# Optimization experiments

Measured on AMD Instinct MI355X. Metric: run time of the kernel, lower is better.

## Reference

```python
import jax, jax.numpy as jnp
import numpy as np

D, C, H, W = 8, 512, 64, 64


def setup_inputs() -> dict:
    key = jax.random.key(0)
    k1, k2, k3 = jax.random.split(key, 3)
    x = jax.random.normal(k1, (D, C, H, W), dtype=jnp.float32)
    atten = jax.random.normal(k2, (D, C, C), dtype=jnp.float32)
    gamma = jax.random.normal(k3, (1,), dtype=jnp.float32)
    return {"x": x, "atten": atten, "gamma": gamma}


def reference(x, atten, gamma):
    d, c, h, w = x.shape
    q = x.reshape(d, c, h * w)              # q == v == flattened x; k = q^T
    # energy[d, i, j] = <channel_i, channel_j> over spatial positions
    energy = jnp.einsum('din,djn->dij', q, q)
    # max-centering: rowmax - energy (note the sign flip vs standard softmax)
    energy_new = jnp.max(energy, axis=-1, keepdims=True) - energy
    attention = jax.nn.softmax(energy_new, axis=-1)
    attention = jax.nn.softmax(attention + atten, axis=-1)
    # out = attention^T @ v : out[d, j, n] = sum_i attention[d, i, j] * v[d, i, n]
    out = jnp.einsum('dij,din->djn', attention, q).reshape(d, c, h, w)
    return gamma * out + x
```

## Files before the change

kernel.cpp:

```cpp
#include <hip/hip_runtime.h>
#include <hip/hip_bf16.h>

#define DD 8
#define CC 512
#define NN 4096
#define SPLITK 4
#define KSP (NN / SPLITK)

typedef __bf16 bf16x8 __attribute__((ext_vector_type(8)));
typedef float  f32x4  __attribute__((ext_vector_type(4)));

__device__ __forceinline__ ushort f2bf(float f) {
  unsigned u = __float_as_uint(f);
  u = (u + 0x7fffu + ((u >> 16) & 1u)) >> 16;
  return (ushort)u;
}
__device__ __forceinline__ float bf2f(ushort h) {
  return __uint_as_float(((unsigned)h) << 16);
}

__device__ __forceinline__ void gl_lds16(const ushort* g, ushort* l) {
  __builtin_amdgcn_global_load_lds(
      (const __attribute__((address_space(1))) void*)g,
      (__attribute__((address_space(3))) void*)l, 16, 0, 0);
}

__global__ __launch_bounds__(256) void k0_convert(
    const float* __restrict__ x, ushort* __restrict__ qh,
    ushort* __restrict__ ql, ushort* __restrict__ qt) {
  int d = blockIdx.z, ct = blockIdx.y, nt = blockIdx.x;
  __shared__ ushort T[64][68];
  int t = threadIdx.x;
  int rr = t >> 4;
  int c4 = (t & 15) * 4;
  const float* xb = x + ((size_t)(d * CC + ct * 64)) * NN + nt * 64;
#pragma unroll
  for (int it = 0; it < 4; ++it) {
    int r = it * 16 + rr;
    float4 v = *(const float4*)(xb + (size_t)r * NN + c4);
    ushort h0 = f2bf(v.x), h1 = f2bf(v.y), h2 = f2bf(v.z), h3 = f2bf(v.w);
    ushort l0 = f2bf(v.x - bf2f(h0)), l1 = f2bf(v.y - bf2f(h1));
    ushort l2 = f2bf(v.z - bf2f(h2)), l3 = f2bf(v.w - bf2f(h3));
    size_t qi = ((size_t)(d * CC + ct * 64 + r)) * NN + nt * 64 + c4;
    *(ushort4*)(qh + qi) = make_ushort4(h0, h1, h2, h3);
    *(ushort4*)(ql + qi) = make_ushort4(l0, l1, l2, l3);
    *(ushort4*)&T[r][c4] = make_ushort4(h0, h1, h2, h3);
  }
  __syncthreads();
#pragma unroll
  for (int it = 0; it < 4; ++it) {
    int nl = it * 16 + rr;
    ushort4 v = make_ushort4(T[c4 + 0][nl], T[c4 + 1][nl], T[c4 + 2][nl], T[c4 + 3][nl]);
    *(ushort4*)(qt + ((size_t)(d * NN + nt * 64 + nl)) * CC + ct * 64 + c4) = v;
  }
}

__global__ __launch_bounds__(256, 2) void k1_gram(
    const ushort* __restrict__ qh, const ushort* __restrict__ ql,
    float* __restrict__ Ep) {
  __shared__ ushort As[2][128 * 32];
  __shared__ ushort Bs[2][128 * 32];
  int b = blockIdx.x;
  int s = b & 3, tmn = (b >> 2) & 15, d = b >> 6;
  int tm = tmn >> 2, tn = tmn & 3;
  int t = threadIdx.x, lane = t & 63, w = t >> 6;
  int wm = (w >> 1) * 64, wn = (w & 1) * 64;
  int qd = lane >> 4, fr = lane & 15;

  const ushort* srcbase = (w & 1) ? ql : qh;
  int rowblk = (w < 2) ? tm : tn;
  const ushort* gsrc = srcbase +
      ((size_t)(d * CC + rowblk * 128 + (lane >> 2))) * NN +
      (size_t)s * KSP + (lane & 3) * 8;
  ushort* ldst = (w < 2) ? As[w & 1] : Bs[w & 1];

  f32x4 acc[4][4];
#pragma unroll
  for (int i = 0; i < 4; ++i)
#pragma unroll
    for (int j = 0; j < 4; ++j) acc[i][j] = (f32x4){0.f, 0.f, 0.f, 0.f};

  for (int kk = 0; kk < KSP / 32; ++kk) {
    __syncthreads();
    const ushort* g0 = gsrc + (size_t)kk * 32;
#pragma unroll
    for (int c = 0; c < 8; ++c)
      gl_lds16(g0 + (size_t)c * 16 * NN, ldst + c * 512);
    __syncthreads();

    bf16x8 ah[4], al[4];
#pragma unroll
    for (int mi = 0; mi < 4; ++mi) {
      int off = (wm + mi * 16 + fr) * 32 + qd * 8;
      ah[mi] = *(const bf16x8*)&As[0][off];
      al[mi] = *(const bf16x8*)&As[1][off];
    }
#pragma unroll
    for (int ni = 0; ni < 4; ++ni) {
      int off = (wn + ni * 16 + fr) * 32 + qd * 8;
      bf16x8 bh = *(const bf16x8*)&Bs[0][off];
      bf16x8 bl = *(const bf16x8*)&Bs[1][off];
#pragma unroll
      for (int mi = 0; mi < 4; ++mi) {
        acc[mi][ni] = __builtin_amdgcn_mfma_f32_16x16x32_bf16(ah[mi], bh, acc[mi][ni], 0, 0, 0);
        acc[mi][ni] = __builtin_amdgcn_mfma_f32_16x16x32_bf16(ah[mi], bl, acc[mi][ni], 0, 0, 0);
        acc[mi][ni] = __builtin_amdgcn_mfma_f32_16x16x32_bf16(al[mi], bh, acc[mi][ni], 0, 0, 0);
      }
    }
  }

  size_t ebase = ((size_t)(s * DD + d)) * ((size_t)CC * CC);
#pragma unroll
  for (int mi = 0; mi < 4; ++mi) {
    int r0 = tm * 128 + wm + mi * 16 + qd * 4;
#pragma unroll
    for (int ni = 0; ni < 4; ++ni) {
      int c0 = tn * 128 + wn + ni * 16 + fr;
      float* ep = Ep + ebase + (size_t)r0 * CC + c0;
#pragma unroll
      for (int r = 0; r < 4; ++r) ep[(size_t)r * CC] = acc[mi][ni][r];
    }
  }
}

__device__ __forceinline__ float bred(float v, float* red, int op) {
#pragma unroll
  for (int o = 32; o > 0; o >>= 1) {
    float other = __shfl_xor(v, o, 64);
    v = (op == 0) ? fminf(v, other) : (op == 1) ? (v + other) : fmaxf(v, other);
  }
  __syncthreads();
  if ((threadIdx.x & 63) == 0) red[threadIdx.x >> 6] = v;
  __syncthreads();
  if (op == 0) return fminf(fminf(red[0], red[1]), fminf(red[2], red[3]));
  if (op == 1) return red[0] + red[1] + red[2] + red[3];
  return fmaxf(fmaxf(red[0], red[1]), fmaxf(red[2], red[3]));
}

__global__ __launch_bounds__(256) void k2_softmax(
    const float* __restrict__ Ep, const float* __restrict__ atten,
    ushort* __restrict__ a2t) {
  int d = blockIdx.y, i0 = blockIdx.x * 16;
  int t = threadIdx.x;
  __shared__ float red[4];
  __shared__ ushort T[512][17];
  const size_t SP = (size_t)DD * CC * CC;
  for (int r = 0; r < 16; ++r) {
    size_t base = ((size_t)(d * CC + i0 + r)) * CC;
    float e0 = Ep[base + t] + Ep[SP + base + t] + Ep[2 * SP + base + t] + Ep[3 * SP + base + t];
    float e1 = Ep[base + t + 256] + Ep[SP + base + t + 256] +
               Ep[2 * SP + base + t + 256] + Ep[3 * SP + base + t + 256];
    float mn = bred(fminf(e0, e1), red, 0);
    float p0 = __expf(mn - e0), p1 = __expf(mn - e1);
    float s1 = bred(p0 + p1, red, 1);
    float inv1 = 1.0f / s1;
    float t0 = p0 * inv1 + atten[base + t];
    float t1 = p1 * inv1 + atten[base + t + 256];
    float mx = bred(fmaxf(t0, t1), red, 2);
    float q0 = __expf(t0 - mx), q1 = __expf(t1 - mx);
    float s2 = bred(q0 + q1, red, 1);
    float inv2 = 1.0f / s2;
    T[t][r] = f2bf(q0 * inv2);
    T[t + 256][r] = f2bf(q1 * inv2);
  }
  __syncthreads();
#pragma unroll
  for (int jj = 0; jj < 2; ++jj) {
    int j = t + jj * 256;
    size_t ob = ((size_t)(d * CC + j)) * CC + i0;
#pragma unroll
    for (int c4 = 0; c4 < 4; ++c4) {
      ushort4 v = make_ushort4(T[j][c4 * 4], T[j][c4 * 4 + 1],
                               T[j][c4 * 4 + 2], T[j][c4 * 4 + 3]);
      *(ushort4*)(a2t + ob + c4 * 4) = v;
    }
  }
}

__global__ __launch_bounds__(256, 2) void k3_out(
    const ushort* __restrict__ a2t, const ushort* __restrict__ qt,
    const float* __restrict__ x, const float* __restrict__ gamma,
    float* __restrict__ out) {
  __shared__ ushort As[128 * 32];
  __shared__ ushort Bs[128 * 32];
  int b = blockIdx.x;
  int nt = b & 31, jt = (b >> 5) & 3, d = b >> 7;
  int t = threadIdx.x, lane = t & 63, w = t >> 6;
  int wm = (w >> 1) * 64, wn = (w & 1) * 64;
  int qd = lane >> 4, fr = lane & 15;

  const ushort* src = (w < 2)
      ? (a2t + (size_t)d * CC * CC + (size_t)(jt * 128) * CC)
      : (qt + (size_t)d * NN * CC + (size_t)(nt * 128) * CC);
  ushort* ldst = (w < 2) ? As : Bs;
  int cbase = (w & 1) * 4;
  const ushort* g0 = src + ((size_t)(cbase * 16 + (lane >> 2))) * CC + (lane & 3) * 8;
  ushort* l0 = ldst + cbase * 16 * 32;

  f32x4 acc[4][4];
#pragma unroll
  for (int i = 0; i < 4; ++i)
#pragma unroll
    for (int j = 0; j < 4; ++j) acc[i][j] = (f32x4){0.f, 0.f, 0.f, 0.f};

  for (int kk = 0; kk < CC / 32; ++kk) {
    __syncthreads();
#pragma unroll
    for (int c = 0; c < 4; ++c)
      gl_lds16(g0 + kk * 32 + (size_t)(c * 16) * CC, l0 + c * 512);
    __syncthreads();

    bf16x8 a[4];
#pragma unroll
    for (int mi = 0; mi < 4; ++mi)
      a[mi] = *(const bf16x8*)&As[(wm + mi * 16 + fr) * 32 + qd * 8];
#pragma unroll
    for (int ni = 0; ni < 4; ++ni) {
      bf16x8 bb = *(const bf16x8*)&Bs[(wn + ni * 16 + fr) * 32 + qd * 8];
#pragma unroll
      for (int mi = 0; mi < 4; ++mi)
        acc[mi][ni] = __builtin_amdgcn_mfma_f32_16x16x32_bf16(a[mi], bb, acc[mi][ni], 0, 0, 0);
    }
  }

  float g = gamma[0];
#pragma unroll
  for (int mi = 0; mi < 4; ++mi) {
    int j0 = jt * 128 + wm + mi * 16 + qd * 4;
#pragma unroll
    for (int ni = 0; ni < 4; ++ni) {
      int n0 = nt * 128 + wn + ni * 16 + fr;
#pragma unroll
      for (int r = 0; r < 4; ++r) {
        size_t idx = ((size_t)(d * CC + j0 + r)) * NN + n0;
        out[idx] = g * acc[mi][ni][r] + x[idx];
      }
    }
  }
}

extern "C" void kernel_launch(void* const* d_in, const int* in_sizes, int n_in,
                              void* d_out, int out_size, void* d_ws, size_t ws_size,
                              hipStream_t stream) {
  (void)in_sizes; (void)n_in; (void)out_size; (void)ws_size;
  const float* x     = (const float*)d_in[0];
  const float* atten = (const float*)d_in[1];
  const float* gamma = (const float*)d_in[2];
  float* out = (float*)d_out;

  char* ws = (char*)d_ws;
  ushort* qh  = (ushort*)(ws);
  ushort* ql  = (ushort*)(ws + 33554432);
  ushort* qt  = (ushort*)(ws + 67108864);
  float*  Ep  = (float*) (ws + 100663296);
  ushort* a2t = (ushort*)(ws + 134217728);

  k0_convert<<<dim3(64, 8, 8), 256, 0, stream>>>(x, qh, ql, qt);
  k1_gram   <<<dim3(512), 256, 0, stream>>>(qh, ql, Ep);
  k2_softmax<<<dim3(32, 8), 256, 0, stream>>>(Ep, atten, a2t);
  k3_out    <<<dim3(1024), 256, 0, stream>>>(a2t, qt, x, gamma, out);
}
```

Measured before the change: 256.6 us.

## Exploit Gram symmetry, adaptive split-K, warp-per-row softmax, vectorized output epilogue

The Gram kernel now computes only the 10 upper-triangular 128x128 tiles per batch and mirrors off-diagonal tiles with a transposed write, roughly halving MFMA work. Split-K depth becomes a runtime parameter, going to 8 when the workspace is large enough, to keep more blocks in flight. The softmax kernel handles one row per wavefront with 8 elements per lane, so it reduces with shuffles only and no block barriers, and it uses vector loads and stores. The output GEMM swaps operand roles so the epilogue does float4 loads of x and float4 stores of out. The costs are more partial-sum traffic when split is 8 and scattered transposed writes for the mirrored tiles.

Result: faster. 235.0 us (-8.4%).

```diff
diff --git a/kernel.cpp b/kernel.cpp
--- a/kernel.cpp
+++ b/kernel.cpp
@@ -4,11 +4,10 @@
 #define DD 8
 #define CC 512
 #define NN 4096
-#define SPLITK 4
-#define KSP (NN / SPLITK)
 
 typedef __bf16 bf16x8 __attribute__((ext_vector_type(8)));
 typedef float  f32x4  __attribute__((ext_vector_type(4)));
+typedef ushort ush8   __attribute__((ext_vector_type(8)));
 
 __device__ __forceinline__ ushort f2bf(float f) {
   unsigned u = __float_as_uint(f);
@@ -57,12 +56,15 @@
 
 __global__ __launch_bounds__(256, 2) void k1_gram(
     const ushort* __restrict__ qh, const ushort* __restrict__ ql,
-    float* __restrict__ Ep) {
+    float* __restrict__ Ep, int ns, int nkk, int ksp) {
   __shared__ ushort As[2][128 * 32];
   __shared__ ushort Bs[2][128 * 32];
   int b = blockIdx.x;
-  int s = b & 3, tmn = (b >> 2) & 15, d = b >> 6;
-  int tm = tmn >> 2, tn = tmn & 3;
+  int s = b % ns;
+  int rem = b / ns;
+  int tile = rem % 10, d = rem / 10;
+  int tm = (int)((0x3221110000ULL >> (tile * 4)) & 15ULL);
+  int tn = (int)((0x3323213210ULL >> (tile * 4)) & 15ULL);
   int t = threadIdx.x, lane = t & 63, w = t >> 6;
   int wm = (w >> 1) * 64, wn = (w & 1) * 64;
   int qd = lane >> 4, fr = lane & 15;
@@ -71,7 +73,7 @@
   int rowblk = (w < 2) ? tm : tn;
   const ushort* gsrc = srcbase +
       ((size_t)(d * CC + rowblk * 128 + (lane >> 2))) * NN +
-      (size_t)s * KSP + (lane & 3) * 8;
+      (size_t)s * ksp + (lane & 3) * 8;
   ushort* ldst = (w < 2) ? As[w & 1] : Bs[w & 1];
 
   f32x4 acc[4][4];
@@ -80,7 +82,7 @@
 #pragma unroll
     for (int j = 0; j < 4; ++j) acc[i][j] = (f32x4){0.f, 0.f, 0.f, 0.f};
 
-  for (int kk = 0; kk < KSP / 32; ++kk) {
+  for (int kk = 0; kk < nkk; ++kk) {
     __syncthreads();
     const ushort* g0 = gsrc + (size_t)kk * 32;
 #pragma unroll
@@ -121,59 +123,96 @@
       for (int r = 0; r < 4; ++r) ep[(size_t)r * CC] = acc[mi][ni][r];
     }
   }
-}
-
-__device__ __forceinline__ float bred(float v, float* red, int op) {
-#pragma unroll
-  for (int o = 32; o > 0; o >>= 1) {
-    float other = __shfl_xor(v, o, 64);
-    v = (op == 0) ? fminf(v, other) : (op == 1) ? (v + other) : fmaxf(v, other);
-  }
-  __syncthreads();
-  if ((threadIdx.x & 63) == 0) red[threadIdx.x >> 6] = v;
-  __syncthreads();
-  if (op == 0) return fminf(fminf(red[0], red[1]), fminf(red[2], red[3]));
-  if (op == 1) return red[0] + red[1] + red[2] + red[3];
-  return fmaxf(fmaxf(red[0], red[1]), fmaxf(red[2], red[3]));
+  if (tm != tn) {
+#pragma unroll
+    for (int mi = 0; mi < 4; ++mi) {
+      int r0 = tm * 128 + wm + mi * 16 + qd * 4;
+#pragma unroll
+      for (int ni = 0; ni < 4; ++ni) {
+        int c0 = tn * 128 + wn + ni * 16 + fr;
+        float4 v = make_float4(acc[mi][ni][0], acc[mi][ni][1],
+                               acc[mi][ni][2], acc[mi][ni][3]);
+        *(float4*)(Ep + ebase + (size_t)c0 * CC + r0) = v;
+      }
+    }
+  }
+}
+
+__device__ __forceinline__ float wmin(float v) {
+#pragma unroll
+  for (int o = 32; o > 0; o >>= 1) v = fminf(v, __shfl_xor(v, o));
+  return v;
+}
+__device__ __forceinline__ float wmax(float v) {
+#pragma unroll
+  for (int o = 32; o > 0; o >>= 1) v = fmaxf(v, __shfl_xor(v, o));
+  return v;
+}
+__device__ __forceinline__ float wsum(float v) {
+#pragma unroll
+  for (int o = 32; o > 0; o >>= 1) v += __shfl_xor(v, o);
+  return v;
 }
 
 __global__ __launch_bounds__(256) void k2_softmax(
     const float* __restrict__ Ep, const float* __restrict__ atten,
-    ushort* __restrict__ a2t) {
-  int d = blockIdx.y, i0 = blockIdx.x * 16;
-  int t = threadIdx.x;
-  __shared__ float red[4];
-  __shared__ ushort T[512][17];
+    ushort* __restrict__ a2t, int ns) {
+  int d = blockIdx.y, i0 = blockIdx.x * 8;
+  int t = threadIdx.x, lane = t & 63, w = t >> 6;
+  int j8 = lane * 8;
+  __shared__ ushort T[8][520];
   const size_t SP = (size_t)DD * CC * CC;
-  for (int r = 0; r < 16; ++r) {
-    size_t base = ((size_t)(d * CC + i0 + r)) * CC;
-    float e0 = Ep[base + t] + Ep[SP + base + t] + Ep[2 * SP + base + t] + Ep[3 * SP + base + t];
-    float e1 = Ep[base + t + 256] + Ep[SP + base + t + 256] +
-               Ep[2 * SP + base + t + 256] + Ep[3 * SP + base + t + 256];
-    float mn = bred(fminf(e0, e1), red, 0);
-    float p0 = __expf(mn - e0), p1 = __expf(mn - e1);
-    float s1 = bred(p0 + p1, red, 1);
+
+#pragma unroll
+  for (int r2 = 0; r2 < 2; ++r2) {
+    int ri = w * 2 + r2;
+    size_t base = ((size_t)(d * CC + i0 + ri)) * CC + j8;
+    f32x4 a0 = (f32x4){0.f, 0.f, 0.f, 0.f};
+    f32x4 a1 = (f32x4){0.f, 0.f, 0.f, 0.f};
+    for (int s = 0; s < ns; ++s) {
+      const float* p = Ep + (size_t)s * SP + base;
+      a0 += *(const f32x4*)p;
+      a1 += *(const f32x4*)(p + 4);
+    }
+    float mn = fminf(fminf(fminf(a0[0], a0[1]), fminf(a0[2], a0[3])),
+                     fminf(fminf(a1[0], a1[1]), fminf(a1[2], a1[3])));
+    mn = wmin(mn);
+    float p0 = __expf(mn - a0[0]), p1 = __expf(mn - a0[1]);
+    float p2 = __expf(mn - a0[2]), p3 = __expf(mn - a0[3]);
+    float p4 = __expf(mn - a1[0]), p5 = __expf(mn - a1[1]);
+    float p6 = __expf(mn - a1[2]), p7 = __expf(mn - a1[3]);
+    float s1 = wsum(p0 + p1 + p2 + p3 + p4 + p5 + p6 + p7);
     float inv1 = 1.0f / s1;
-    float t0 = p0 * inv1 + atten[base + t];
-    float t1 = p1 * inv1 + atten[base + t + 256];
-    float mx = bred(fmaxf(t0, t1), red, 2);
-    float q0 = __expf(t0 - mx), q1 = __expf(t1 - mx);
-    float s2 = bred(q0 + q1, red, 1);
+    const float* ap = atten + base;
+    f32x4 t0 = *(const f32x4*)ap;
+    f32x4 t1 = *(const f32x4*)(ap + 4);
+    float u0 = p0 * inv1 + t0[0], u1 = p1 * inv1 + t0[1];
+    float u2 = p2 * inv1 + t0[2], u3 = p3 * inv1 + t0[3];
+    float u4 = p4 * inv1 + t1[0], u5 = p5 * inv1 + t1[1];
+    float u6 = p6 * inv1 + t1[2], u7 = p7 * inv1 + t1[3];
+    float mx = wmax(fmaxf(fmaxf(fmaxf(u0, u1), fmaxf(u2, u3)),
+                          fmaxf(fmaxf(u4, u5), fmaxf(u6, u7))));
+    float q0 = __expf(u0 - mx), q1 = __expf(u1 - mx);
+    float q2 = __expf(u2 - mx), q3 = __expf(u3 - mx);
+    float q4 = __expf(u4 - mx), q5 = __expf(u5 - mx);
+    float q6 = __expf(u6 - mx), q7 = __expf(u7 - mx);
+    float s2 = wsum(q0 + q1 + q2 + q3 + q4 + q5 + q6 + q7);
     float inv2 = 1.0f / s2;
-    T[t][r] = f2bf(q0 * inv2);
-    T[t + 256][r] = f2bf(q1 * inv2);
+    ush8 o;
+    o[0] = f2bf(q0 * inv2); o[1] = f2bf(q1 * inv2);
+    o[2] = f2bf(q2 * inv2); o[3] = f2bf(q3 * inv2);
+    o[4] = f2bf(q4 * inv2); o[5] = f2bf(q5 * inv2);
+    o[6] = f2bf(q6 * inv2); o[7] = f2bf(q7 * inv2);
+    *(ush8*)&T[ri][j8] = o;
   }
   __syncthreads();
 #pragma unroll
-  for (int jj = 0; jj < 2; ++jj) {
-    int j = t + jj * 256;
-    size_t ob = ((size_t)(d * CC + j)) * CC + i0;
-#pragma unroll
-    for (int c4 = 0; c4 < 4; ++c4) {
-      ushort4 v = make_ushort4(T[j][c4 * 4], T[j][c4 * 4 + 1],
-                               T[j][c4 * 4 + 2], T[j][c4 * 4 + 3]);
-      *(ushort4*)(a2t + ob + c4 * 4) = v;
-    }
+  for (int it = 0; it < 2; ++it) {
+    int j = t + it * 256;
+    ush8 o;
+#pragma unroll
+    for (int k = 0; k < 8; ++k) o[k] = T[k][j];
+    *(ush8*)&a2t[((size_t)(d * CC + j)) * CC + i0] = o;
   }
 }
 
@@ -186,7 +225,7 @@
   int b = blockIdx.x;
   int nt = b & 31, jt = (b >> 5) & 3, d = b >> 7;
   int t = threadIdx.x, lane = t & 63, w = t >> 6;
-  int wm = (w >> 1) * 64, wn = (w & 1) * 64;
+  int wj = (w >> 1) * 64, wn2 = (w & 1) * 64;
   int qd = lane >> 4, fr = lane & 15;
 
   const ushort* src = (w < 2)
@@ -210,31 +249,33 @@
       gl_lds16(g0 + kk * 32 + (size_t)(c * 16) * CC, l0 + c * 512);
     __syncthreads();
 
-    bf16x8 a[4];
-#pragma unroll
-    for (int mi = 0; mi < 4; ++mi)
-      a[mi] = *(const bf16x8*)&As[(wm + mi * 16 + fr) * 32 + qd * 8];
-#pragma unroll
-    for (int ni = 0; ni < 4; ++ni) {
-      bf16x8 bb = *(const bf16x8*)&Bs[(wn + ni * 16 + fr) * 32 + qd * 8];
-#pragma unroll
-      for (int mi = 0; mi < 4; ++mi)
-        acc[mi][ni] = __builtin_amdgcn_mfma_f32_16x16x32_bf16(a[mi], bb, acc[mi][ni], 0, 0, 0);
+    bf16x8 qf[4];
+#pragma unroll
+    for (int ii = 0; ii < 4; ++ii)
+      qf[ii] = *(const bf16x8*)&Bs[(wn2 + ii * 16 + fr) * 32 + qd * 8];
+#pragma unroll
+    for (int jj = 0; jj < 4; ++jj) {
+      bf16x8 af = *(const bf16x8*)&As[(wj + jj * 16 + fr) * 32 + qd * 8];
+#pragma unroll
+      for (int ii = 0; ii < 4; ++ii)
+        acc[ii][jj] = __builtin_amdgcn_mfma_f32_16x16x32_bf16(qf[ii], af, acc[ii][jj], 0, 0, 0);
     }
   }
 
   float g = gamma[0];
 #pragma unroll
-  for (int mi = 0; mi < 4; ++mi) {
-    int j0 = jt * 128 + wm + mi * 16 + qd * 4;
-#pragma unroll
-    for (int ni = 0; ni < 4; ++ni) {
-      int n0 = nt * 128 + wn + ni * 16 + fr;
-#pragma unroll
-      for (int r = 0; r < 4; ++r) {
-        size_t idx = ((size_t)(d * CC + j0 + r)) * NN + n0;
-        out[idx] = g * acc[mi][ni][r] + x[idx];
-      }
+  for (int ii = 0; ii < 4; ++ii) {
+    int n0 = nt * 128 + wn2 + ii * 16 + qd * 4;
+#pragma unroll
+    for (int jj = 0; jj < 4; ++jj) {
+      int j = jt * 128 + wj + jj * 16 + fr;
+      size_t idx = ((size_t)(d * CC + j)) * NN + n0;
+      float4 xv = *(const float4*)(x + idx);
+      float4 ov = make_float4(g * acc[ii][jj][0] + xv.x,
+                              g * acc[ii][jj][1] + xv.y,
+                              g * acc[ii][jj][2] + xv.z,
+                              g * acc[ii][jj][3] + xv.w);
+      *(float4*)(out + idx) = ov;
     }
   }
 }
@@ -242,7 +283,7 @@
 extern "C" void kernel_launch(void* const* d_in, const int* in_sizes, int n_in,
                               void* d_out, int out_size, void* d_ws, size_t ws_size,
                               hipStream_t stream) {
-  (void)in_sizes; (void)n_in; (void)out_size; (void)ws_size;
+  (void)in_sizes; (void)n_in; (void)out_size;
   const float* x     = (const float*)d_in[0];
   const float* atten = (const float*)d_in[1];
   const float* gamma = (const float*)d_in[2];
@@ -252,11 +293,15 @@
   ushort* qh  = (ushort*)(ws);
   ushort* ql  = (ushort*)(ws + 33554432);
   ushort* qt  = (ushort*)(ws + 67108864);
-  float*  Ep  = (float*) (ws + 100663296);
-  ushort* a2t = (ushort*)(ws + 134217728);
+  ushort* a2t = (ushort*)(ws + 100663296);
+  float*  Ep  = (float*) (ws + 104857600);
+
+  int ns = (ws_size >= 104857600ULL + 8ULL * 8388608ULL) ? 8 : 4;
+  int ksp = NN / ns;
+  int nkk = ksp / 32;
 
   k0_convert<<<dim3(64, 8, 8), 256, 0, stream>>>(x, qh, ql, qt);
-  k1_gram   <<<dim3(512), 256, 0, stream>>>(qh, ql, Ep);
-  k2_softmax<<<dim3(32, 8), 256, 0, stream>>>(Ep, atten, a2t);
+  k1_gram   <<<dim3(80 * ns), 256, 0, stream>>>(qh, ql, Ep, ns, nkk, ksp);
+  k2_softmax<<<dim3(64, 8), 256, 0, stream>>>(Ep, atten, a2t, ns);
   k3_out    <<<dim3(1024), 256, 0, stream>>>(a2t, qt, x, gamma, out);
 }
```
